# Performance work log

Hardware: AMD Instinct MI355X
Metric: run time of the kernel (lower is better)

The kernel has to match this reference:

```python
import jax, jax.numpy as jnp
import numpy as np

N_NODES = 50000
N_EDGES = 800000
IN_DIM = 128
HIDDEN = 256
N_ETYPES = 13
N_STEPS = 6
NUM_GRAPHS = 64


def setup_inputs() -> dict:
    key = jax.random.key(0)
    ks = jax.random.split(key, 10)
    feat = jax.random.normal(ks[0], (N_NODES, IN_DIM), dtype=jnp.float32)
    W = jax.random.normal(ks[1], (N_ETYPES, HIDDEN, HIDDEN), dtype=jnp.float32) * 0.05
    W_ih = jax.random.normal(ks[2], (3 * HIDDEN, HIDDEN), dtype=jnp.float32) * 0.05
    W_hh = jax.random.normal(ks[3], (3 * HIDDEN, HIDDEN), dtype=jnp.float32) * 0.05
    b_ih = jnp.zeros((3 * HIDDEN,), dtype=jnp.float32)
    b_hh = jnp.zeros((3 * HIDDEN,), dtype=jnp.float32)
    Wc = jax.random.normal(ks[4], (1, HIDDEN), dtype=jnp.float32) * 0.05
    bc = jnp.zeros((1,), dtype=jnp.float32)
    src = jax.random.randint(ks[5], (N_EDGES,), 0, N_NODES, dtype=jnp.int32)
    dst = jax.random.randint(ks[6], (N_EDGES,), 0, N_NODES, dtype=jnp.int32)
    etype = jax.random.randint(ks[7], (N_EDGES,), 0, N_ETYPES, dtype=jnp.int32)
    graph_id = jnp.sort(jax.random.randint(ks[8], (N_NODES,), 0, NUM_GRAPHS, dtype=jnp.int32))
    return {"feat": feat, "W": W, "W_ih": W_ih, "W_hh": W_hh, "b_ih": b_ih,
            "b_hh": b_hh, "Wc": Wc, "bc": bc, "src": src, "dst": dst,
            "etype": etype, "graph_id": graph_id}


def reference(feat, W, W_ih, W_hh, b_ih, b_hh, Wc, bc, src, dst, etype, graph_id):
    N, H = feat.shape[0], W.shape[-1]
    # zero-pad input features to hidden size (DGL GatedGraphConv behaviour)
    h0 = jnp.concatenate([feat, jnp.zeros((N, H - feat.shape[1]), feat.dtype)], axis=1)

    def step(h, _):
        # per-etype linear transform of all nodes: [n_etypes, N, H]
        Th = jnp.einsum('nd,edf->enf', h, W)
        # gather transformed source feature per edge by its edge type: [E, H]
        msg = Th[etype, src]
        # scatter-sum aggregation into destination nodes: [N, H]
        a = jax.ops.segment_sum(msg, dst, num_segments=N)
        # torch.nn.GRUCell(a, h)
        gx = a @ W_ih.T + b_ih
        gh = h @ W_hh.T + b_hh
        xr, xz, xn = jnp.split(gx, 3, axis=-1)
        hr, hz, hn = jnp.split(gh, 3, axis=-1)
        r = jax.nn.sigmoid(xr + hr)
        z = jax.nn.sigmoid(xz + hz)
        n = jnp.tanh(xn + r * hn)
        return (1.0 - z) * n + z * h, None

    h, _ = jax.lax.scan(step, h0, None, length=N_STEPS)
    h = jax.nn.relu(h)
    # dgl.sum_nodes readout per graph: [num_graphs, H]
    hg = jax.ops.segment_sum(h, graph_id, num_segments=NUM_GRAPHS)
    out = jax.nn.sigmoid(hg @ Wc.T + bc)
    return out.squeeze(-1)
```

## Files before the change

### kernel.cpp

```cpp
#include <hip/hip_runtime.h>
#include <math.h>

#define N_NODES   50000
#define N_EDGES   800000
#define IN_DIM    128
#define HIDDEN    256
#define N_ETYPES  13
#define N_STEPS   6
#define NUM_GRAPHS 64
#define NKEYS     (N_ETYPES * N_NODES)
#define SCAN_T    512

typedef __attribute__((ext_vector_type(8))) short bf16x8;
typedef __attribute__((ext_vector_type(4))) float f32x4;

__global__ __launch_bounds__(256) void k_init_h(const float* __restrict__ feat,
                                                float* __restrict__ h) {
    int i = blockIdx.x * 256 + threadIdx.x;
    if (i >= N_NODES * 64) return;
    int v = i >> 6;
    int q = i & 63;
    float4 val;
    if (q < 32) val = ((const float4*)(feat + (size_t)v * IN_DIM))[q];
    else        val = make_float4(0.f, 0.f, 0.f, 0.f);
    ((float4*)(h + (size_t)v * HIDDEN))[q] = val;
}

__global__ __launch_bounds__(256) void k_splitW(const float* __restrict__ W,
                                                short* __restrict__ Whi,
                                                short* __restrict__ Wlo) {
    int i = blockIdx.x * 256 + threadIdx.x;
    if (i >= N_ETYPES * 65536) return;
    int t = i >> 16, rem = i & 65535, n = rem >> 8, k = rem & 255;
    float x = W[(size_t)t * 65536 + k * 256 + n];
    unsigned u = __float_as_uint(x);
    unsigned short hb = (unsigned short)(u >> 16);
    float hf = __uint_as_float((unsigned)hb << 16);
    float l = x - hf;
    unsigned short lb = (unsigned short)(__float_as_uint(l) >> 16);
    Whi[i] = (short)hb;
    Wlo[i] = (short)lb;
}

__global__ __launch_bounds__(256) void k_splitLin(const float* __restrict__ Wsrc,
                                                  short* __restrict__ hi,
                                                  short* __restrict__ lo, int n) {
    int i = blockIdx.x * 256 + threadIdx.x;
    if (i >= n) return;
    float x = Wsrc[i];
    unsigned u = __float_as_uint(x);
    unsigned short hb = (unsigned short)(u >> 16);
    float hf = __uint_as_float((unsigned)hb << 16);
    float l = x - hf;
    unsigned short lb = (unsigned short)(__float_as_uint(l) >> 16);
    hi[i] = (short)hb;
    lo[i] = (short)lb;
}

__global__ __launch_bounds__(256) void k_hist(const int* __restrict__ dst,
                                              const int* __restrict__ et,
                                              int* __restrict__ counts) {
    int e = blockIdx.x * 256 + threadIdx.x;
    if (e >= N_EDGES) return;
    int key = et[e] * N_NODES + dst[e];
    atomicAdd(&counts[key], 1);
}

__global__ __launch_bounds__(SCAN_T) void k_scan1(const int* __restrict__ in,
                                                  int* __restrict__ lexcl,
                                                  int* __restrict__ bsums, int n) {
    __shared__ int s[SCAN_T];
    int i = blockIdx.x * SCAN_T + threadIdx.x;
    int v = (i < n) ? in[i] : 0;
    s[threadIdx.x] = v;
    __syncthreads();
    for (int off = 1; off < SCAN_T; off <<= 1) {
        int t = (threadIdx.x >= off) ? s[threadIdx.x - off] : 0;
        __syncthreads();
        s[threadIdx.x] += t;
        __syncthreads();
    }
    if (i < n) lexcl[i] = s[threadIdx.x] - v;
    if (threadIdx.x == SCAN_T - 1) bsums[blockIdx.x] = s[SCAN_T - 1];
}

__global__ __launch_bounds__(256) void k_scan2(int* __restrict__ bsums, int nb,
                                               int* __restrict__ ptr) {
    __shared__ int s[256];
    int tid = threadIdx.x;
    const int C = (nb + 255) / 256;
    int vals[8];
    int base = tid * C;
    int sum = 0;
    for (int i = 0; i < C; ++i) {
        int idx = base + i;
        int v = (idx < nb) ? bsums[idx] : 0;
        vals[i] = sum;
        sum += v;
    }
    s[tid] = sum;
    __syncthreads();
    int own = sum;
    for (int off = 1; off < 256; off <<= 1) {
        int t = (tid >= off) ? s[tid - off] : 0;
        __syncthreads();
        s[tid] += t;
        __syncthreads();
    }
    int exclBlk = s[tid] - own;
    for (int i = 0; i < C; ++i) {
        int idx = base + i;
        if (idx < nb) bsums[idx] = exclBlk + vals[i];
    }
    if (tid == 0) ptr[NKEYS] = N_EDGES;
}

__global__ __launch_bounds__(SCAN_T) void k_scan3(const int* __restrict__ lexcl,
                                                  const int* __restrict__ bsums,
                                                  int* __restrict__ ptr, int n) {
    int i = blockIdx.x * SCAN_T + threadIdx.x;
    if (i < n) ptr[i] = lexcl[i] + bsums[blockIdx.x];
}

__global__ __launch_bounds__(256) void k_place(const int* __restrict__ dst,
                                               const int* __restrict__ et,
                                               const int* __restrict__ src,
                                               int* __restrict__ cursor,
                                               unsigned* __restrict__ ebuf) {
    int e = blockIdx.x * 256 + threadIdx.x;
    if (e >= N_EDGES) return;
    int d = dst[e];
    int key = et[e] * N_NODES + d;
    int pos = atomicAdd(&cursor[key], 1);
    ebuf[pos] = ((unsigned)d << 16) | (unsigned)src[e];
}

__device__ __forceinline__ void split8(const float4& A, const float4& B,
                                       bf16x8& hi, bf16x8& lo) {
    float x[8] = {A.x, A.y, A.z, A.w, B.x, B.y, B.z, B.w};
    #pragma unroll
    for (int e = 0; e < 8; ++e) {
        unsigned u = __float_as_uint(x[e]);
        unsigned short hb = (unsigned short)(u >> 16);
        float hf = __uint_as_float((unsigned)hb << 16);
        float l = x[e] - hf;
        unsigned short lb = (unsigned short)(__float_as_uint(l) >> 16);
        hi[e] = (short)hb;
        lo[e] = (short)lb;
    }
}

__global__ __launch_bounds__(256, 4) void k_msg(const unsigned* __restrict__ ebuf,
                                                const int* __restrict__ ptr,
                                                const float* __restrict__ h,
                                                const short* __restrict__ Whi,
                                                const short* __restrict__ Wlo,
                                                float* __restrict__ a) {
    __shared__ float4 Sh4[32 * 64];
    const int br   = blockIdx.x * 32;
    const int tid  = threadIdx.x;
    const int l    = tid & 63;
    const int w    = tid >> 6;
    const int ln15 = l & 15;
    const int lhi  = l >> 4;
    const int g    = tid >> 4;
    const int q    = tid & 15;
    const float4* h4 = (const float4*)h;
    float* shf = (float*)Sh4;

    f32x4 acc[2][4] = {};

    for (int t = 0; t < N_ETYPES; ++t) {
        float4 z4 = make_float4(0.f, 0.f, 0.f, 0.f);
        #pragma unroll
        for (int i = 0; i < 8; ++i) Sh4[tid + i * 256] = z4;
        __syncthreads();
        {
            int base = t * N_NODES + br;
            int endk = (br + 32 <= N_NODES) ? (base + 32) : (t * N_NODES + N_NODES);
            int beg  = ptr[base];
            int end  = ptr[endk];
            for (int i = beg + g; i < end; i += 16) {
                unsigned pk = ebuf[i];
                int s = (int)(pk & 0xFFFFu);
                int r = (int)(pk >> 16) - br;
                int sw = r & 7;
                #pragma unroll
                for (int j = 0; j < 4; ++j) {
                    float4 v = h4[(size_t)s * 64 + j * 16 + q];
                    int jj = (j * 16 + q) ^ sw;
                    float* p = shf + ((r * 64 + jj) << 2);
                    atomicAdd(p + 0, v.x);
                    atomicAdd(p + 1, v.y);
                    atomicAdd(p + 2, v.z);
                    atomicAdd(p + 3, v.w);
                }
            }
        }
        __syncthreads();
        const short* WH = Whi + ((size_t)t << 16);
        const short* WL = Wlo + ((size_t)t << 16);
        #pragma unroll 2
        for (int K0 = 0; K0 < 8; ++K0) {
            bf16x8 bh[4], bl[4];
            #pragma unroll
            for (int cb = 0; cb < 4; ++cb) {
                int col = (w << 6) + (cb << 4) + ln15;
                size_t off = (size_t)col * 256 + (K0 << 5) + (lhi << 3);
                bh[cb] = *reinterpret_cast<const bf16x8*>(WH + off);
                bl[cb] = *reinterpret_cast<const bf16x8*>(WL + off);
            }
            #pragma unroll
            for (int rf = 0; rf < 2; ++rf) {
                int row = (rf << 4) + ln15;
                int j0  = (K0 << 3) + (lhi << 1);
                int sw  = row & 7;
                float4 a0 = Sh4[row * 64 + (j0 ^ sw)];
                float4 a1 = Sh4[row * 64 + ((j0 + 1) ^ sw)];
                bf16x8 ah, al;
                split8(a0, a1, ah, al);
                #pragma unroll
                for (int cb = 0; cb < 4; ++cb) {
                    acc[rf][cb] = __builtin_amdgcn_mfma_f32_16x16x32_bf16(ah, bh[cb], acc[rf][cb], 0, 0, 0);
                    acc[rf][cb] = __builtin_amdgcn_mfma_f32_16x16x32_bf16(ah, bl[cb], acc[rf][cb], 0, 0, 0);
                    acc[rf][cb] = __builtin_amdgcn_mfma_f32_16x16x32_bf16(al, bh[cb], acc[rf][cb], 0, 0, 0);
                }
            }
        }
        __syncthreads();
    }
    #pragma unroll
    for (int rf = 0; rf < 2; ++rf) {
        #pragma unroll
        for (int m = 0; m < 4; ++m) {
            int row = br + (rf << 4) + (lhi << 2) + m;
            if (row < N_NODES) {
                #pragma unroll
                for (int cb = 0; cb < 4; ++cb) {
                    int col = (w << 6) + (cb << 4) + ln15;
                    a[(size_t)row * 256 + col] = acc[rf][cb][m];
                }
            }
        }
    }
}

__device__ __forceinline__ float sigm(float x) { return 1.0f / (1.0f + expf(-x)); }

__global__ __launch_bounds__(256, 2) void k_gru(const float* __restrict__ a,
                                                const float* __restrict__ h,
                                                const short* __restrict__ WihH,
                                                const short* __restrict__ WihL,
                                                const short* __restrict__ WhhH,
                                                const short* __restrict__ WhhL,
                                                const float* __restrict__ b_ih,
                                                const float* __restrict__ b_hh,
                                                float* __restrict__ hN) {
    const int br   = blockIdx.x * 64;
    const int f0   = blockIdx.y * 64;
    const int tid  = threadIdx.x;
    const int w    = tid >> 6;
    const int l    = tid & 63;
    const int ln15 = l & 15;
    const int lhi  = l >> 4;

    f32x4 accx[3][4] = {};
    f32x4 acch[3][4] = {};

    int rowA = br + (w << 4) + ln15;
    if (rowA >= N_NODES) rowA = N_NODES - 1;
    const float* aRow = a + (size_t)rowA * 256;
    const float* hRow = h + (size_t)rowA * 256;

    #pragma unroll 2
    for (int K0 = 0; K0 < 8; ++K0) {
        const int koff = (K0 << 5) + (lhi << 3);
        float4 av0 = *(const float4*)(aRow + koff);
        float4 av1 = *(const float4*)(aRow + koff + 4);
        float4 hv0 = *(const float4*)(hRow + koff);
        float4 hv1 = *(const float4*)(hRow + koff + 4);
        bf16x8 aH, aL, hH, hL;
        split8(av0, av1, aH, aL);
        split8(hv0, hv1, hH, hL);
        #pragma unroll
        for (int g = 0; g < 3; ++g) {
            #pragma unroll
            for (int cb = 0; cb < 4; ++cb) {
                int col = g * 256 + f0 + (cb << 4) + ln15;
                size_t off = (size_t)col * 256 + koff;
                bf16x8 bH = *reinterpret_cast<const bf16x8*>(WihH + off);
                bf16x8 bL = *reinterpret_cast<const bf16x8*>(WihL + off);
                accx[g][cb] = __builtin_amdgcn_mfma_f32_16x16x32_bf16(aH, bH, accx[g][cb], 0, 0, 0);
                accx[g][cb] = __builtin_amdgcn_mfma_f32_16x16x32_bf16(aH, bL, accx[g][cb], 0, 0, 0);
                accx[g][cb] = __builtin_amdgcn_mfma_f32_16x16x32_bf16(aL, bH, accx[g][cb], 0, 0, 0);
                bH = *reinterpret_cast<const bf16x8*>(WhhH + off);
                bL = *reinterpret_cast<const bf16x8*>(WhhL + off);
                acch[g][cb] = __builtin_amdgcn_mfma_f32_16x16x32_bf16(hH, bH, acch[g][cb], 0, 0, 0);
                acch[g][cb] = __builtin_amdgcn_mfma_f32_16x16x32_bf16(hH, bL, acch[g][cb], 0, 0, 0);
                acch[g][cb] = __builtin_amdgcn_mfma_f32_16x16x32_bf16(hL, bH, acch[g][cb], 0, 0, 0);
            }
        }
    }
    #pragma unroll
    for (int cb = 0; cb < 4; ++cb) {
        int f = f0 + (cb << 4) + ln15;
        float bxr = b_ih[f], bxz = b_ih[256 + f], bxn = b_ih[512 + f];
        float bhr = b_hh[f], bhz = b_hh[256 + f], bhn = b_hh[512 + f];
        #pragma unroll
        for (int m = 0; m < 4; ++m) {
            int row = br + (w << 4) + (lhi << 2) + m;
            if (row >= N_NODES) continue;
            float hv = h[(size_t)row * 256 + f];
            float r = sigm(accx[0][cb][m] + bxr + acch[0][cb][m] + bhr);
            float z = sigm(accx[1][cb][m] + bxz + acch[1][cb][m] + bhz);
            float n = tanhf(accx[2][cb][m] + bxn + r * (acch[2][cb][m] + bhn));
            hN[(size_t)row * 256 + f] = (1.f - z) * n + z * hv;
        }
    }
}

__global__ __launch_bounds__(256) void k_readout1(const float* __restrict__ h,
                                                  const int* __restrict__ gid,
                                                  float* __restrict__ hg) {
    int row0 = blockIdx.x * 32;
    if (row0 >= N_NODES) return;
    int f = threadIdx.x;
    int end = row0 + 32; if (end > N_NODES) end = N_NODES;
    float acc = 0.f;
    int cur = gid[row0];
    for (int r = row0; r < end; ++r) {
        int g = gid[r];
        if (g != cur) {
            atomicAdd(&hg[cur * HIDDEN + f], acc);
            acc = 0.f; cur = g;
        }
        float x = h[(size_t)r * HIDDEN + f];
        acc += (x > 0.f) ? x : 0.f;
    }
    atomicAdd(&hg[cur * HIDDEN + f], acc);
}

__global__ __launch_bounds__(256) void k_readout2(const float* __restrict__ hg,
                                                  const float* __restrict__ Wc,
                                                  const float* __restrict__ bc,
                                                  float* __restrict__ out) {
    __shared__ float s[256];
    int g = blockIdx.x;
    int f = threadIdx.x;
    s[f] = hg[g * HIDDEN + f] * Wc[f];
    __syncthreads();
    for (int off = 128; off > 0; off >>= 1) {
        if (f < off) s[f] += s[f + off];
        __syncthreads();
    }
    if (f == 0) out[g] = 1.0f / (1.0f + expf(-(s[0] + bc[0])));
}

extern "C" void kernel_launch(void* const* d_in, const int* in_sizes, int n_in,
                              void* d_out, int out_size, void* d_ws, size_t ws_size,
                              hipStream_t stream) {
    const float* feat  = (const float*)d_in[0];
    const float* W     = (const float*)d_in[1];
    const float* W_ih  = (const float*)d_in[2];
    const float* W_hh  = (const float*)d_in[3];
    const float* b_ih  = (const float*)d_in[4];
    const float* b_hh  = (const float*)d_in[5];
    const float* Wc    = (const float*)d_in[6];
    const float* bc    = (const float*)d_in[7];
    const int*   src   = (const int*)d_in[8];
    const int*   dst   = (const int*)d_in[9];
    const int*   etype = (const int*)d_in[10];
    const int*   gid   = (const int*)d_in[11];
    float* out = (float*)d_out;

    char* ws = (char*)d_ws;
    size_t off = 0;
    auto alloc = [&](size_t bytes) {
        void* p = ws + off;
        off += (bytes + 255) & ~(size_t)255;
        return p;
    };
    float* hA   = (float*)alloc((size_t)N_NODES * HIDDEN * 4);
    float* hB   = (float*)alloc((size_t)N_NODES * HIDDEN * 4);
    float* a    = (float*)alloc((size_t)N_NODES * HIDDEN * 4);
    int* bufA   = (int*)alloc((size_t)(NKEYS + 1) * 4);
    int* bufB   = (int*)alloc((size_t)NKEYS * 4);
    unsigned* ebuf = (unsigned*)alloc((size_t)N_EDGES * 4);
    int* bsums  = (int*)alloc((size_t)2048 * 4);
    float* hg   = (float*)alloc((size_t)NUM_GRAPHS * HIDDEN * 4);
    short* Whi  = (short*)alloc((size_t)N_ETYPES * 65536 * 2);
    short* Wlo  = (short*)alloc((size_t)N_ETYPES * 65536 * 2);
    short* WihH = (short*)alloc((size_t)768 * 256 * 2);
    short* WihL = (short*)alloc((size_t)768 * 256 * 2);
    short* WhhH = (short*)alloc((size_t)768 * 256 * 2);
    short* WhhL = (short*)alloc((size_t)768 * 256 * 2);
    (void)ws_size; (void)n_in; (void)in_sizes; (void)out_size;

    const int SCAN_BLOCKS = (NKEYS + SCAN_T - 1) / SCAN_T;
    const int NLIN = 768 * 256;

    hipMemsetAsync(bufA, 0, (size_t)NKEYS * 4, stream);
    k_hist<<<(N_EDGES + 255) / 256, 256, 0, stream>>>(dst, etype, bufA);
    k_scan1<<<SCAN_BLOCKS, SCAN_T, 0, stream>>>(bufA, bufB, bsums, NKEYS);
    k_scan2<<<1, 256, 0, stream>>>(bsums, SCAN_BLOCKS, bufA);
    k_scan3<<<SCAN_BLOCKS, SCAN_T, 0, stream>>>(bufB, bsums, bufA, NKEYS);
    hipMemcpyAsync(bufB, bufA, (size_t)NKEYS * 4, hipMemcpyDeviceToDevice, stream);
    k_place<<<(N_EDGES + 255) / 256, 256, 0, stream>>>(dst, etype, src, bufB, ebuf);

    k_splitW<<<(N_ETYPES * 65536 + 255) / 256, 256, 0, stream>>>(W, Whi, Wlo);
    k_splitLin<<<(NLIN + 255) / 256, 256, 0, stream>>>(W_ih, WihH, WihL, NLIN);
    k_splitLin<<<(NLIN + 255) / 256, 256, 0, stream>>>(W_hh, WhhH, WhhL, NLIN);
    k_init_h<<<(N_NODES * 64 + 255) / 256, 256, 0, stream>>>(feat, hA);

    float* hc = hA;
    float* hn = hB;
    const dim3 gMsg((N_NODES + 31) / 32, 1);
    const dim3 gGru((N_NODES + 63) / 64, HIDDEN / 64);

    for (int step = 0; step < N_STEPS; ++step) {
        k_msg<<<gMsg, 256, 0, stream>>>(ebuf, bufA, hc, Whi, Wlo, a);
        k_gru<<<gGru, 256, 0, stream>>>(a, hc, WihH, WihL, WhhH, WhhL,
                                        b_ih, b_hh, hn);
        float* tmp = hc; hc = hn; hn = tmp;
    }

    hipMemsetAsync(hg, 0, (size_t)NUM_GRAPHS * HIDDEN * 4, stream);
    k_readout1<<<(N_NODES + 31) / 32, 256, 0, stream>>>(hc, gid, hg);
    k_readout2<<<NUM_GRAPHS, 256, 0, stream>>>(hg, Wc, bc, out);
}
```

Before: 13.93 ms.

## Store hidden state as pre-split bf16 hi/lo plus fp16 copy for gathers

The hidden state is now stored as a bf16 hi/lo pair plus a separate fp16 copy, replacing fp32. The message kernel gathers fp16 source rows, halving gather bytes per edge. The GRU kernel reads the pre-split hi/lo directly instead of splitting fp32 on the fly, and its grid order is swapped so the feature-column blocks of one row tile run adjacently. The cost is reduced precision in the aggregated messages (fp16) and three output writes per element in the GRU.

Result: no change. 14.12 ms (+1.3%).

```diff
diff --git a/kernel.cpp b/kernel.cpp
--- a/kernel.cpp
+++ b/kernel.cpp
@@ -13,9 +13,24 @@
 
 typedef __attribute__((ext_vector_type(8))) short bf16x8;
 typedef __attribute__((ext_vector_type(4))) float f32x4;
+typedef __attribute__((ext_vector_type(4))) unsigned short u16x4;
+typedef __attribute__((ext_vector_type(8))) _Float16 f16x8;
+typedef __attribute__((ext_vector_type(4))) _Float16 f16x4;
+
+__device__ __forceinline__ float bf2f(unsigned short u) {
+    return __uint_as_float((unsigned)u << 16);
+}
+__device__ __forceinline__ void fsplit(float x, unsigned short& hi, unsigned short& lo) {
+    unsigned u = __float_as_uint(x);
+    hi = (unsigned short)(u >> 16);
+    float l = x - __uint_as_float((u >> 16) << 16);
+    lo = (unsigned short)(__float_as_uint(l) >> 16);
+}
 
 __global__ __launch_bounds__(256) void k_init_h(const float* __restrict__ feat,
-                                                float* __restrict__ h) {
+                                                unsigned short* __restrict__ hHi,
+                                                unsigned short* __restrict__ hLo,
+                                                _Float16* __restrict__ hF16) {
     int i = blockIdx.x * 256 + threadIdx.x;
     if (i >= N_NODES * 64) return;
     int v = i >> 6;
@@ -23,7 +38,20 @@
     float4 val;
     if (q < 32) val = ((const float4*)(feat + (size_t)v * IN_DIM))[q];
     else        val = make_float4(0.f, 0.f, 0.f, 0.f);
-    ((float4*)(h + (size_t)v * HIDDEN))[q] = val;
+    unsigned short h0, l0, h1, l1, h2, l2, h3, l3;
+    fsplit(val.x, h0, l0);
+    fsplit(val.y, h1, l1);
+    fsplit(val.z, h2, l2);
+    fsplit(val.w, h3, l3);
+    u16x4 hi4, lo4;
+    hi4[0] = h0; hi4[1] = h1; hi4[2] = h2; hi4[3] = h3;
+    lo4[0] = l0; lo4[1] = l1; lo4[2] = l2; lo4[3] = l3;
+    *(u16x4*)(hHi + (size_t)v * 256 + q * 4) = hi4;
+    *(u16x4*)(hLo + (size_t)v * 256 + q * 4) = lo4;
+    f16x4 f4;
+    f4[0] = (_Float16)val.x; f4[1] = (_Float16)val.y;
+    f4[2] = (_Float16)val.z; f4[3] = (_Float16)val.w;
+    *(f16x4*)(hF16 + (size_t)v * 256 + q * 4) = f4;
 }
 
 __global__ __launch_bounds__(256) void k_splitW(const float* __restrict__ W,
@@ -33,11 +61,8 @@
     if (i >= N_ETYPES * 65536) return;
     int t = i >> 16, rem = i & 65535, n = rem >> 8, k = rem & 255;
     float x = W[(size_t)t * 65536 + k * 256 + n];
-    unsigned u = __float_as_uint(x);
-    unsigned short hb = (unsigned short)(u >> 16);
-    float hf = __uint_as_float((unsigned)hb << 16);
-    float l = x - hf;
-    unsigned short lb = (unsigned short)(__float_as_uint(l) >> 16);
+    unsigned short hb, lb;
+    fsplit(x, hb, lb);
     Whi[i] = (short)hb;
     Wlo[i] = (short)lb;
 }
@@ -47,12 +72,8 @@
                                                   short* __restrict__ lo, int n) {
     int i = blockIdx.x * 256 + threadIdx.x;
     if (i >= n) return;
-    float x = Wsrc[i];
-    unsigned u = __float_as_uint(x);
-    unsigned short hb = (unsigned short)(u >> 16);
-    float hf = __uint_as_float((unsigned)hb << 16);
-    float l = x - hf;
-    unsigned short lb = (unsigned short)(__float_as_uint(l) >> 16);
+    unsigned short hb, lb;
+    fsplit(Wsrc[i], hb, lb);
     hi[i] = (short)hb;
     lo[i] = (short)lb;
 }
@@ -140,11 +161,8 @@
     float x[8] = {A.x, A.y, A.z, A.w, B.x, B.y, B.z, B.w};
     #pragma unroll
     for (int e = 0; e < 8; ++e) {
-        unsigned u = __float_as_uint(x[e]);
-        unsigned short hb = (unsigned short)(u >> 16);
-        float hf = __uint_as_float((unsigned)hb << 16);
-        float l = x[e] - hf;
-        unsigned short lb = (unsigned short)(__float_as_uint(l) >> 16);
+        unsigned short hb, lb;
+        fsplit(x[e], hb, lb);
         hi[e] = (short)hb;
         lo[e] = (short)lb;
     }
@@ -152,7 +170,7 @@
 
 __global__ __launch_bounds__(256, 4) void k_msg(const unsigned* __restrict__ ebuf,
                                                 const int* __restrict__ ptr,
-                                                const float* __restrict__ h,
+                                                const _Float16* __restrict__ hF16,
                                                 const short* __restrict__ Whi,
                                                 const short* __restrict__ Wlo,
                                                 float* __restrict__ a) {
@@ -165,7 +183,6 @@
     const int lhi  = l >> 4;
     const int g    = tid >> 4;
     const int q    = tid & 15;
-    const float4* h4 = (const float4*)h;
     float* shf = (float*)Sh4;
 
     f32x4 acc[2][4] = {};
@@ -186,14 +203,21 @@
                 int r = (int)(pk >> 16) - br;
                 int sw = r & 7;
                 #pragma unroll
-                for (int j = 0; j < 4; ++j) {
-                    float4 v = h4[(size_t)s * 64 + j * 16 + q];
-                    int jj = (j * 16 + q) ^ sw;
-                    float* p = shf + ((r * 64 + jj) << 2);
-                    atomicAdd(p + 0, v.x);
-                    atomicAdd(p + 1, v.y);
-                    atomicAdd(p + 2, v.z);
-                    atomicAdd(p + 3, v.w);
+                for (int j2 = 0; j2 < 2; ++j2) {
+                    const _Float16* vp = hF16 + (size_t)s * 256 + j2 * 128 + q * 8;
+                    f16x8 v8 = *reinterpret_cast<const f16x8*>(vp);
+                    int c0 = (j2 * 32 + 2 * q) ^ sw;
+                    int c1 = (j2 * 32 + 2 * q + 1) ^ sw;
+                    float* p0 = shf + ((r * 64 + c0) << 2);
+                    float* p1 = shf + ((r * 64 + c1) << 2);
+                    atomicAdd(p0 + 0, (float)v8[0]);
+                    atomicAdd(p0 + 1, (float)v8[1]);
+                    atomicAdd(p0 + 2, (float)v8[2]);
+                    atomicAdd(p0 + 3, (float)v8[3]);
+                    atomicAdd(p1 + 0, (float)v8[4]);
+                    atomicAdd(p1 + 1, (float)v8[5]);
+                    atomicAdd(p1 + 2, (float)v8[6]);
+                    atomicAdd(p1 + 3, (float)v8[7]);
                 }
             }
         }
@@ -248,16 +272,19 @@
 __device__ __forceinline__ float sigm(float x) { return 1.0f / (1.0f + expf(-x)); }
 
 __global__ __launch_bounds__(256, 2) void k_gru(const float* __restrict__ a,
-                                                const float* __restrict__ h,
+                                                const unsigned short* __restrict__ hHi,
+                                                const unsigned short* __restrict__ hLo,
                                                 const short* __restrict__ WihH,
                                                 const short* __restrict__ WihL,
                                                 const short* __restrict__ WhhH,
                                                 const short* __restrict__ WhhL,
                                                 const float* __restrict__ b_ih,
                                                 const float* __restrict__ b_hh,
-                                                float* __restrict__ hN) {
-    const int br   = blockIdx.x * 64;
-    const int f0   = blockIdx.y * 64;
+                                                unsigned short* __restrict__ hNHi,
+                                                unsigned short* __restrict__ hNLo,
+                                                _Float16* __restrict__ hNF16) {
+    const int f0   = blockIdx.x * 64;
+    const int br   = blockIdx.y * 64;
     const int tid  = threadIdx.x;
     const int w    = tid >> 6;
     const int l    = tid & 63;
@@ -270,18 +297,18 @@
     int rowA = br + (w << 4) + ln15;
     if (rowA >= N_NODES) rowA = N_NODES - 1;
     const float* aRow = a + (size_t)rowA * 256;
-    const float* hRow = h + (size_t)rowA * 256;
+    const unsigned short* hHiRow = hHi + (size_t)rowA * 256;
+    const unsigned short* hLoRow = hLo + (size_t)rowA * 256;
 
     #pragma unroll 2
     for (int K0 = 0; K0 < 8; ++K0) {
         const int koff = (K0 << 5) + (lhi << 3);
         float4 av0 = *(const float4*)(aRow + koff);
         float4 av1 = *(const float4*)(aRow + koff + 4);
-        float4 hv0 = *(const float4*)(hRow + koff);
-        float4 hv1 = *(const float4*)(hRow + koff + 4);
-        bf16x8 aH, aL, hH, hL;
+        bf16x8 aH, aL;
         split8(av0, av1, aH, aL);
-        split8(hv0, hv1, hH, hL);
+        bf16x8 hH = *reinterpret_cast<const bf16x8*>(hHiRow + koff);
+        bf16x8 hL = *reinterpret_cast<const bf16x8*>(hLoRow + koff);
         #pragma unroll
         for (int g = 0; g < 3; ++g) {
             #pragma unroll
@@ -310,16 +337,23 @@
         for (int m = 0; m < 4; ++m) {
             int row = br + (w << 4) + (lhi << 2) + m;
             if (row >= N_NODES) continue;
-            float hv = h[(size_t)row * 256 + f];
+            size_t idx = (size_t)row * 256 + f;
+            float hv = bf2f(hHi[idx]) + bf2f(hLo[idx]);
             float r = sigm(accx[0][cb][m] + bxr + acch[0][cb][m] + bhr);
             float z = sigm(accx[1][cb][m] + bxz + acch[1][cb][m] + bhz);
             float n = tanhf(accx[2][cb][m] + bxn + r * (acch[2][cb][m] + bhn));
-            hN[(size_t)row * 256 + f] = (1.f - z) * n + z * hv;
-        }
-    }
-}
-
-__global__ __launch_bounds__(256) void k_readout1(const float* __restrict__ h,
+            float o = (1.f - z) * n + z * hv;
+            unsigned short ohi, olo;
+            fsplit(o, ohi, olo);
+            hNHi[idx] = ohi;
+            hNLo[idx] = olo;
+            hNF16[idx] = (_Float16)o;
+        }
+    }
+}
+
+__global__ __launch_bounds__(256) void k_readout1(const unsigned short* __restrict__ hHi,
+                                                  const unsigned short* __restrict__ hLo,
                                                   const int* __restrict__ gid,
                                                   float* __restrict__ hg) {
     int row0 = blockIdx.x * 32;
@@ -334,7 +368,8 @@
             atomicAdd(&hg[cur * HIDDEN + f], acc);
             acc = 0.f; cur = g;
         }
-        float x = h[(size_t)r * HIDDEN + f];
+        size_t idx = (size_t)r * HIDDEN + f;
+        float x = bf2f(hHi[idx]) + bf2f(hLo[idx]);
         acc += (x > 0.f) ? x : 0.f;
     }
     atomicAdd(&hg[cur * HIDDEN + f], acc);
@@ -380,8 +415,11 @@
         off += (bytes + 255) & ~(size_t)255;
         return p;
     };
-    float* hA   = (float*)alloc((size_t)N_NODES * HIDDEN * 4);
-    float* hB   = (float*)alloc((size_t)N_NODES * HIDDEN * 4);
+    unsigned short* hHiA = (unsigned short*)alloc((size_t)N_NODES * HIDDEN * 2);
+    unsigned short* hLoA = (unsigned short*)alloc((size_t)N_NODES * HIDDEN * 2);
+    unsigned short* hHiB = (unsigned short*)alloc((size_t)N_NODES * HIDDEN * 2);
+    unsigned short* hLoB = (unsigned short*)alloc((size_t)N_NODES * HIDDEN * 2);
+    _Float16* hF16 = (_Float16*)alloc((size_t)N_NODES * HIDDEN * 2);
     float* a    = (float*)alloc((size_t)N_NODES * HIDDEN * 4);
     int* bufA   = (int*)alloc((size_t)(NKEYS + 1) * 4);
     int* bufB   = (int*)alloc((size_t)NKEYS * 4);
@@ -410,21 +448,22 @@
     k_splitW<<<(N_ETYPES * 65536 + 255) / 256, 256, 0, stream>>>(W, Whi, Wlo);
     k_splitLin<<<(NLIN + 255) / 256, 256, 0, stream>>>(W_ih, WihH, WihL, NLIN);
     k_splitLin<<<(NLIN + 255) / 256, 256, 0, stream>>>(W_hh, WhhH, WhhL, NLIN);
-    k_init_h<<<(N_NODES * 64 + 255) / 256, 256, 0, stream>>>(feat, hA);
-
-    float* hc = hA;
-    float* hn = hB;
+    k_init_h<<<(N_NODES * 64 + 255) / 256, 256, 0, stream>>>(feat, hHiA, hLoA, hF16);
+
+    unsigned short* hcHi = hHiA; unsigned short* hcLo = hLoA;
+    unsigned short* hnHi = hHiB; unsigned short* hnLo = hLoB;
     const dim3 gMsg((N_NODES + 31) / 32, 1);
-    const dim3 gGru((N_NODES + 63) / 64, HIDDEN / 64);
+    const dim3 gGru(HIDDEN / 64, (N_NODES + 63) / 64);
 
     for (int step = 0; step < N_STEPS; ++step) {
-        k_msg<<<gMsg, 256, 0, stream>>>(ebuf, bufA, hc, Whi, Wlo, a);
-        k_gru<<<gGru, 256, 0, stream>>>(a, hc, WihH, WihL, WhhH, WhhL,
-                                        b_ih, b_hh, hn);
-        float* tmp = hc; hc = hn; hn = tmp;
+        k_msg<<<gMsg, 256, 0, stream>>>(ebuf, bufA, hF16, Whi, Wlo, a);
+        k_gru<<<gGru, 256, 0, stream>>>(a, hcHi, hcLo, WihH, WihL, WhhH, WhhL,
+                                        b_ih, b_hh, hnHi, hnLo, hF16);
+        unsigned short* t1 = hcHi; hcHi = hnHi; hnHi = t1;
+        unsigned short* t2 = hcLo; hcLo = hnLo; hnLo = t2;
     }
 
     hipMemsetAsync(hg, 0, (size_t)NUM_GRAPHS * HIDDEN * 4, stream);
-    k_readout1<<<(N_NODES + 31) / 32, 256, 0, stream>>>(hc, gid, hg);
+    k_readout1<<<(N_NODES + 31) / 32, 256, 0, stream>>>(hcHi, hcLo, gid, hg);
     k_readout2<<<NUM_GRAPHS, 256, 0, stream>>>(hg, Wc, bc, out);
 }
```
